# Kernel optimization log

Hardware: AMD Instinct MI355X
Metric: run time of the kernel (lower is better)

## Reference

```python
import jax, jax.numpy as jnp
import numpy as np


def setup_inputs() -> dict:
    key = jax.random.key(0)
    k1, k2 = jax.random.split(key)
    B, Tq, Tk, D = 8, 2048, 2048, 1024
    decoder_hidden = jax.random.normal(k1, (B, Tq, D), dtype=jnp.float32)
    encoder_outputs = jax.random.normal(k2, (B, Tk, D), dtype=jnp.float32)
    return {"decoder_hidden": decoder_hidden, "encoder_outputs": encoder_outputs}


def reference(decoder_hidden, encoder_outputs):
    # scores: [B, Tq, Tk] = decoder_hidden @ encoder_outputs^T (no scaling, as in source)
    scores = jnp.einsum("bqd,bkd->bqk", decoder_hidden, encoder_outputs)
    attention_weights = jax.nn.softmax(scores, axis=2)
    # context: [B, Tq, D]
    context_vector = jnp.einsum("bqk,bkd->bqd", attention_weights, encoder_outputs)
    return (context_vector, attention_weights)
```

## Files before the change

### kernel.cpp

```cpp
#include <hip/hip_runtime.h>


typedef _Float16 f16;
typedef _Float16 half4 __attribute__((ext_vector_type(4)));
typedef _Float16 half8 __attribute__((ext_vector_type(8)));
typedef float floatx16 __attribute__((ext_vector_type(16)));

#define BM 128
#define BN 128
#define BK 64

__device__ __forceinline__ void gl2lds16(const void* g, void* l) {
    __builtin_amdgcn_global_load_lds(
        (const __attribute__((address_space(1))) unsigned int*)g,
        (__attribute__((address_space(3))) unsigned int*)l,
        16, 0, 0);
}

__global__ __launch_bounds__(256) void cvt_f32_f16(const float* __restrict__ src,
                                                   f16* __restrict__ dst, int n4) {
    int i = blockIdx.x * 256 + threadIdx.x;
    if (i >= n4) return;
    float4 v = ((const float4*)src)[i];
    half4 h;
    h[0] = (f16)v.x; h[1] = (f16)v.y; h[2] = (f16)v.z; h[3] = (f16)v.w;
    ((half4*)dst)[i] = h;
}

__global__ __launch_bounds__(256) void k_cvt_transpose(const float* __restrict__ K,
                                                       f16* __restrict__ Kh,
                                                       f16* __restrict__ Kt) {
    __shared__ f16 tile[64][72];
    const int b  = blockIdx.z;
    const int k0 = blockIdx.y * 64;
    const int d0 = blockIdx.x * 64;
    const float* src = K + (size_t)b * 2048 * 1024;
    f16* khb = Kh + (size_t)b * 2048 * 1024;
    f16* ktb = Kt + (size_t)b * 1024 * 2048;
    const int r  = threadIdx.x >> 4;
    const int c4 = (threadIdx.x & 15) * 4;
    #pragma unroll
    for (int it = 0; it < 4; it++) {
        int kr = it * 16 + r;
        float4 v = *(const float4*)&src[(size_t)(k0 + kr) * 1024 + d0 + c4];
        half4 h;
        h[0] = (f16)v.x; h[1] = (f16)v.y; h[2] = (f16)v.z; h[3] = (f16)v.w;
        *(half4*)&khb[(size_t)(k0 + kr) * 1024 + d0 + c4] = h;
        *(half4*)&tile[kr][c4] = h;
    }
    __syncthreads();
    #pragma unroll
    for (int it = 0; it < 4; it++) {
        int dr = it * 16 + r;
        half4 h;
        h[0] = tile[c4 + 0][dr]; h[1] = tile[c4 + 1][dr];
        h[2] = tile[c4 + 2][dr]; h[3] = tile[c4 + 3][dr];
        *(half4*)&ktb[(size_t)(d0 + dr) * 2048 + k0 + c4] = h;
    }
}

__global__ __launch_bounds__(256) void gemm_bt(const f16* __restrict__ Amat,
                                               const f16* __restrict__ Bmat,
                                               float* __restrict__ C,
                                               int K_, int N, int nN,
                                               long sA, long sB, long sC) {
    __shared__ f16 As[BM * BK];
    __shared__ f16 Bs[BN * BK];
    const int tid  = threadIdx.x;
    const int lane = tid & 63;
    const int wave = tid >> 6;
    const int wm = (wave & 1) * 64;
    const int wn = (wave >> 1) * 64;
    const int bz = blockIdx.x;
    const int tileM = (blockIdx.y / nN) * BM;
    const int tileN = (blockIdx.y % nN) * BN;
    const f16* Ab = Amat + (size_t)bz * sA;
    const f16* Bb = Bmat + (size_t)bz * sB;
    float* Cb = C + (size_t)bz * sC;

    floatx16 acc[2][2];
    #pragma unroll
    for (int t = 0; t < 2; t++)
        #pragma unroll
        for (int u = 0; u < 2; u++)
            #pragma unroll
            for (int r = 0; r < 16; r++) acc[t][u][r] = 0.f;

    const int l31 = lane & 31;
    const int khalf = lane >> 5;
    const int sw = lane & 7;

    for (int k0 = 0; k0 < K_; k0 += BK) {
        #pragma unroll
        for (int r = 0; r < 4; r++) {
            int h = r * 256 + tid;
            int row = h >> 3, cc = h & 7;
            int gcc = cc ^ (row & 7);
            gl2lds16(Ab + (size_t)(tileM + row) * K_ + k0 + gcc * 8, &As[h * 8]);
        }
        #pragma unroll
        for (int r = 0; r < 4; r++) {
            int h = r * 256 + tid;
            int row = h >> 3, cc = h & 7;
            int gcc = cc ^ (row & 7);
            gl2lds16(Bb + (size_t)(tileN + row) * K_ + k0 + gcc * 8, &Bs[h * 8]);
        }
        __syncthreads();

        #pragma unroll
        for (int s = 0; s < 4; s++) {
            const int pc = (s * 2 + khalf) ^ sw;
            half8 af[2], bf[2];
            #pragma unroll
            for (int t = 0; t < 2; t++)
                af[t] = *(const half8*)&As[(wm + t * 32 + l31) * BK + pc * 8];
            #pragma unroll
            for (int u = 0; u < 2; u++)
                bf[u] = *(const half8*)&Bs[(wn + u * 32 + l31) * BK + pc * 8];
            #pragma unroll
            for (int t = 0; t < 2; t++)
                #pragma unroll
                for (int u = 0; u < 2; u++)
                    acc[t][u] = __builtin_amdgcn_mfma_f32_32x32x16_f16(af[t], bf[u], acc[t][u], 0, 0, 0);
        }
        __syncthreads();
    }

    #pragma unroll
    for (int t = 0; t < 2; t++) {
        #pragma unroll
        for (int u = 0; u < 2; u++) {
            int col = tileN + wn + u * 32 + l31;
            int rbase = tileM + wm + t * 32 + 4 * khalf;
            #pragma unroll
            for (int r = 0; r < 16; r++) {
                int row = rbase + (r & 3) + 8 * (r >> 2);
                Cb[(size_t)row * N + col] = acc[t][u][r];
            }
        }
    }
}

__global__ __launch_bounds__(256) void softmax_rows(float* __restrict__ S,
                                                    f16* __restrict__ Wh) {
    const size_t row = blockIdx.x;
    float* p = S + row * 2048;
    f16* ph = Wh + row * 2048;
    const int tid = threadIdx.x;
    const int lane = tid & 63;
    const int wave = tid >> 6;
    __shared__ float red[8];

    float4 va = ((const float4*)p)[tid];
    float4 vb = ((const float4*)p)[tid + 256];
    float m = fmaxf(fmaxf(fmaxf(va.x, va.y), fmaxf(va.z, va.w)),
                    fmaxf(fmaxf(vb.x, vb.y), fmaxf(vb.z, vb.w)));
    #pragma unroll
    for (int off = 32; off; off >>= 1) m = fmaxf(m, __shfl_xor(m, off));
    if (lane == 0) red[wave] = m;
    __syncthreads();
    m = fmaxf(fmaxf(red[0], red[1]), fmaxf(red[2], red[3]));

    va.x = __expf(va.x - m); va.y = __expf(va.y - m);
    va.z = __expf(va.z - m); va.w = __expf(va.w - m);
    vb.x = __expf(vb.x - m); vb.y = __expf(vb.y - m);
    vb.z = __expf(vb.z - m); vb.w = __expf(vb.w - m);
    float s = va.x + va.y + va.z + va.w + vb.x + vb.y + vb.z + vb.w;
    #pragma unroll
    for (int off = 32; off; off >>= 1) s += __shfl_xor(s, off);
    if (lane == 0) red[4 + wave] = s;
    __syncthreads();
    s = red[4] + red[5] + red[6] + red[7];
    float inv = 1.0f / s;
    va.x *= inv; va.y *= inv; va.z *= inv; va.w *= inv;
    vb.x *= inv; vb.y *= inv; vb.z *= inv; vb.w *= inv;
    ((float4*)p)[tid] = va;
    ((float4*)p)[tid + 256] = vb;
    half4 ha, hb;
    ha[0] = (f16)va.x; ha[1] = (f16)va.y; ha[2] = (f16)va.z; ha[3] = (f16)va.w;
    hb[0] = (f16)vb.x; hb[1] = (f16)vb.y; hb[2] = (f16)vb.z; hb[3] = (f16)vb.w;
    ((half4*)ph)[tid] = ha;
    ((half4*)ph)[tid + 256] = hb;
}

extern "C" void kernel_launch(void* const* d_in, const int* in_sizes, int n_in,
                              void* d_out, int out_size, void* d_ws, size_t ws_size,
                              hipStream_t stream) {
    const float* Q = (const float*)d_in[0];
    const float* K = (const float*)d_in[1];
    float* ctx = (float*)d_out;
    float* W   = (float*)d_out + 16777216;

    f16* Qh = (f16*)d_ws;
    f16* Kh = Qh + 16777216;
    f16* Kt = Kh + 16777216;
    f16* Wh = (f16*)d_ws;

    cvt_f32_f16<<<16384, 256, 0, stream>>>(Q, Qh, 4194304);
    k_cvt_transpose<<<dim3(16, 32, 8), 256, 0, stream>>>(K, Kh, Kt);

    gemm_bt<<<dim3(8, 256), 256, 0, stream>>>(
        Qh, Kh, W, 1024, 2048, 16, 2048L * 1024, 2048L * 1024, 2048L * 2048);

    softmax_rows<<<16384, 256, 0, stream>>>(W, Wh);

    gemm_bt<<<dim3(8, 128), 256, 0, stream>>>(
        Wh, Kt, ctx, 2048, 1024, 8, 2048L * 2048, 1024L * 2048, 2048L * 1024);
}
```

Before: 479.9 us.

## Replace GEMM with 256x256 tile, 8-wave, double-buffered pipelined MFMA kernel

```diff
diff --git a/kernel.cpp b/kernel.cpp
--- a/kernel.cpp
+++ b/kernel.cpp
@@ -5,10 +5,6 @@
 typedef _Float16 half4 __attribute__((ext_vector_type(4)));
 typedef _Float16 half8 __attribute__((ext_vector_type(8)));
 typedef float floatx16 __attribute__((ext_vector_type(16)));
-
-#define BM 128
-#define BN 128
-#define BK 64
 
 __device__ __forceinline__ void gl2lds16(const void* g, void* l) {
     __builtin_amdgcn_global_load_lds(
@@ -16,6 +12,8 @@
         (__attribute__((address_space(3))) unsigned int*)l,
         16, 0, 0);
 }
+
+#define MFMA(a, b, c) __builtin_amdgcn_mfma_f32_32x32x16_f16((a), (b), (c), 0, 0, 0)
 
 __global__ __launch_bounds__(256) void cvt_f32_f16(const float* __restrict__ src,
                                                    f16* __restrict__ dst, int n4) {
@@ -59,83 +57,155 @@
     }
 }
 
-__global__ __launch_bounds__(256) void gemm_bt(const f16* __restrict__ Amat,
-                                               const f16* __restrict__ Bmat,
-                                               float* __restrict__ C,
-                                               int K_, int N, int nN,
-                                               long sA, long sB, long sC) {
-    __shared__ f16 As[BM * BK];
-    __shared__ f16 Bs[BN * BK];
+__global__ __launch_bounds__(512) void gemm_bt8(const f16* __restrict__ Amat,
+                                                const f16* __restrict__ Bmat,
+                                                float* __restrict__ C,
+                                                int K_, int N, int nN,
+                                                long sA, long sB, long sC) {
+    __shared__ __align__(16) f16 LA[2][2][8192];
+    __shared__ __align__(16) f16 LB[2][2][8192];
     const int tid  = threadIdx.x;
     const int lane = tid & 63;
     const int wave = tid >> 6;
-    const int wm = (wave & 1) * 64;
-    const int wn = (wave >> 1) * 64;
-    const int bz = blockIdx.x;
-    const int tileM = (blockIdx.y / nN) * BM;
-    const int tileN = (blockIdx.y % nN) * BN;
+    const int wm   = wave >> 2;
+    const int wn   = wave & 3;
+    const int bz   = blockIdx.x;
+    const int tileM = (blockIdx.y / nN) * 256;
+    const int tileN = (blockIdx.y % nN) * 256;
     const f16* Ab = Amat + (size_t)bz * sA;
     const f16* Bb = Bmat + (size_t)bz * sB;
     float* Cb = C + (size_t)bz * sC;
-
-    floatx16 acc[2][2];
-    #pragma unroll
-    for (int t = 0; t < 2; t++)
-        #pragma unroll
-        for (int u = 0; u < 2; u++)
+    const int NT = K_ >> 6;
+
+    const int r0  = tid >> 3;
+    const int gcc = (tid & 7) ^ (r0 & 7);
+    const f16* sAp = Ab + (size_t)(tileM + r0) * K_ + gcc * 8;
+    const f16* sBp = Bb + (size_t)(tileN + (r0 & 31) + (r0 >> 5) * 64) * K_ + gcc * 8;
+
+    const int r31 = lane & 31;
+    const int kh  = lane >> 5;
+    const int sw  = lane & 7;
+
+    floatx16 acc[4][2];
+    #pragma unroll
+    for (int f = 0; f < 4; f++)
+        #pragma unroll
+        for (int g = 0; g < 2; g++)
             #pragma unroll
-            for (int r = 0; r < 16; r++) acc[t][u][r] = 0.f;
-
-    const int l31 = lane & 31;
-    const int khalf = lane >> 5;
-    const int sw = lane & 7;
-
-    for (int k0 = 0; k0 < K_; k0 += BK) {
-        #pragma unroll
-        for (int r = 0; r < 4; r++) {
-            int h = r * 256 + tid;
-            int row = h >> 3, cc = h & 7;
-            int gcc = cc ^ (row & 7);
-            gl2lds16(Ab + (size_t)(tileM + row) * K_ + k0 + gcc * 8, &As[h * 8]);
-        }
-        #pragma unroll
-        for (int r = 0; r < 4; r++) {
-            int h = r * 256 + tid;
-            int row = h >> 3, cc = h & 7;
-            int gcc = cc ^ (row & 7);
-            gl2lds16(Bb + (size_t)(tileN + row) * K_ + k0 + gcc * 8, &Bs[h * 8]);
-        }
-        __syncthreads();
-
-        #pragma unroll
-        for (int s = 0; s < 4; s++) {
-            const int pc = (s * 2 + khalf) ^ sw;
-            half8 af[2], bf[2];
-            #pragma unroll
-            for (int t = 0; t < 2; t++)
-                af[t] = *(const half8*)&As[(wm + t * 32 + l31) * BK + pc * 8];
-            #pragma unroll
-            for (int u = 0; u < 2; u++)
-                bf[u] = *(const half8*)&Bs[(wn + u * 32 + l31) * BK + pc * 8];
-            #pragma unroll
-            for (int t = 0; t < 2; t++)
-                #pragma unroll
-                for (int u = 0; u < 2; u++)
-                    acc[t][u] = __builtin_amdgcn_mfma_f32_32x32x16_f16(af[t], bf[u], acc[t][u], 0, 0, 0);
-        }
-        __syncthreads();
-    }
-
-    #pragma unroll
-    for (int t = 0; t < 2; t++) {
-        #pragma unroll
-        for (int u = 0; u < 2; u++) {
-            int col = tileN + wn + u * 32 + l31;
-            int rbase = tileM + wm + t * 32 + 4 * khalf;
+            for (int r = 0; r < 16; r++) acc[f][g][r] = 0.f;
+
+    auto STAGE_A = [&](int par, int h, int T) {
+        const f16* s = sAp + (size_t)(h * 64) * K_ + T * 64;
+        f16* d = &LA[par][h][tid * 8];
+        gl2lds16(s, d);
+        gl2lds16(s + (size_t)128 * K_, d + 4096);
+    };
+    auto STAGE_B = [&](int par, int h, int T) {
+        const f16* s = sBp + (size_t)(h * 32) * K_ + T * 64;
+        f16* d = &LB[par][h][tid * 8];
+        gl2lds16(s, d);
+        gl2lds16(s + (size_t)128 * K_, d + 4096);
+    };
+    auto LDA = [&](int par, int f, int ks) -> half8 {
+        int lr = ((f & 1) << 5) + r31 + (wm << 6);
+        int pc = ((ks << 1) + kh) ^ sw;
+        return *(const half8*)&LA[par][f >> 1][lr * 64 + pc * 8];
+    };
+    auto LDB = [&](int par, int g, int ks) -> half8 {
+        int lr = (wn << 5) + r31;
+        int pc = ((ks << 1) + kh) ^ sw;
+        return *(const half8*)&LB[par][g][lr * 64 + pc * 8];
+    };
+
+    STAGE_A(0, 0, 0); STAGE_B(0, 0, 0); STAGE_A(0, 1, 0); STAGE_B(0, 1, 0);
+    STAGE_A(1, 0, 1); STAGE_B(1, 0, 1); STAGE_A(1, 1, 1);
+    asm volatile("s_waitcnt vmcnt(6)" ::: "memory");
+    __builtin_amdgcn_s_barrier();
+
+    half8 af[2][4], bfa[4], bfb[4];
+    for (int T = 0; T < NT; ++T) {
+        const int par = T & 1, nxt = par ^ 1;
+        #pragma unroll
+        for (int ks = 0; ks < 4; ks++) {
+            af[0][ks] = LDA(par, 0, ks);
+            af[1][ks] = LDA(par, 1, ks);
+            bfa[ks]   = LDB(par, 0, ks);
+        }
+        if (T + 1 < NT) STAGE_B(nxt, 1, T + 1);
+        asm volatile("s_waitcnt lgkmcnt(8)" ::: "memory");
+        __builtin_amdgcn_s_barrier();
+        asm volatile("s_waitcnt lgkmcnt(0)" ::: "memory");
+        __builtin_amdgcn_sched_barrier(0);
+        __builtin_amdgcn_s_setprio(1);
+        #pragma unroll
+        for (int ks = 0; ks < 4; ks++) {
+            acc[0][0] = MFMA(af[0][ks], bfa[ks], acc[0][0]);
+            acc[1][0] = MFMA(af[1][ks], bfa[ks], acc[1][0]);
+        }
+        __builtin_amdgcn_s_setprio(0);
+        __builtin_amdgcn_sched_barrier(0);
+        __builtin_amdgcn_s_barrier();
+        #pragma unroll
+        for (int ks = 0; ks < 4; ks++) bfb[ks] = LDB(par, 1, ks);
+        if (T + 2 < NT) STAGE_A(par, 0, T + 2);
+        __builtin_amdgcn_s_barrier();
+        asm volatile("s_waitcnt lgkmcnt(0)" ::: "memory");
+        __builtin_amdgcn_sched_barrier(0);
+        __builtin_amdgcn_s_setprio(1);
+        #pragma unroll
+        for (int ks = 0; ks < 4; ks++) {
+            acc[0][1] = MFMA(af[0][ks], bfb[ks], acc[0][1]);
+            acc[1][1] = MFMA(af[1][ks], bfb[ks], acc[1][1]);
+        }
+        __builtin_amdgcn_s_setprio(0);
+        __builtin_amdgcn_sched_barrier(0);
+        __builtin_amdgcn_s_barrier();
+        #pragma unroll
+        for (int ks = 0; ks < 4; ks++) {
+            af[0][ks] = LDA(par, 2, ks);
+            af[1][ks] = LDA(par, 3, ks);
+        }
+        if (T + 2 < NT) STAGE_B(par, 0, T + 2);
+        __builtin_amdgcn_s_barrier();
+        asm volatile("s_waitcnt lgkmcnt(0)" ::: "memory");
+        __builtin_amdgcn_sched_barrier(0);
+        __builtin_amdgcn_s_setprio(1);
+        #pragma unroll
+        for (int ks = 0; ks < 4; ks++) {
+            acc[2][1] = MFMA(af[0][ks], bfb[ks], acc[2][1]);
+            acc[3][1] = MFMA(af[1][ks], bfb[ks], acc[3][1]);
+        }
+        __builtin_amdgcn_s_setprio(0);
+        __builtin_amdgcn_sched_barrier(0);
+        __builtin_amdgcn_s_barrier();
+        if (T + 2 < NT) {
+            STAGE_A(par, 1, T + 2);
+            asm volatile("s_waitcnt vmcnt(6)" ::: "memory");
+        } else {
+            asm volatile("s_waitcnt vmcnt(0)" ::: "memory");
+        }
+        __builtin_amdgcn_s_barrier();
+        __builtin_amdgcn_s_setprio(1);
+        #pragma unroll
+        for (int ks = 0; ks < 4; ks++) {
+            acc[2][0] = MFMA(af[0][ks], bfa[ks], acc[2][0]);
+            acc[3][0] = MFMA(af[1][ks], bfa[ks], acc[3][0]);
+        }
+        __builtin_amdgcn_s_setprio(0);
+        __builtin_amdgcn_sched_barrier(0);
+        __builtin_amdgcn_s_barrier();
+    }
+
+    #pragma unroll
+    for (int f = 0; f < 4; f++) {
+        #pragma unroll
+        for (int g = 0; g < 2; g++) {
+            int col   = tileN + (wn << 6) + (g << 5) + r31;
+            int rbase = tileM + (wm << 7) + (f << 5) + (kh << 2);
             #pragma unroll
             for (int r = 0; r < 16; r++) {
-                int row = rbase + (r & 3) + 8 * (r >> 2);
-                Cb[(size_t)row * N + col] = acc[t][u][r];
+                int row = rbase + (r & 3) + ((r >> 2) << 3);
+                Cb[(size_t)row * N + col] = acc[f][g][r];
             }
         }
     }
@@ -199,11 +269,11 @@
     cvt_f32_f16<<<16384, 256, 0, stream>>>(Q, Qh, 4194304);
     k_cvt_transpose<<<dim3(16, 32, 8), 256, 0, stream>>>(K, Kh, Kt);
 
-    gemm_bt<<<dim3(8, 256), 256, 0, stream>>>(
-        Qh, Kh, W, 1024, 2048, 16, 2048L * 1024, 2048L * 1024, 2048L * 2048);
+    gemm_bt8<<<dim3(8, 64), 512, 0, stream>>>(
+        Qh, Kh, W, 1024, 2048, 8, 2048L * 1024, 2048L * 1024, 2048L * 2048);
 
     softmax_rows<<<16384, 256, 0, stream>>>(W, Wh);
 
-    gemm_bt<<<dim3(8, 128), 256, 0, stream>>>(
-        Wh, Kt, ctx, 2048, 1024, 8, 2048L * 2048, 1024L * 2048, 2048L * 1024);
-}
+    gemm_bt8<<<dim3(8, 32), 512, 0, stream>>>(
+        Wh, Kt, ctx, 2048, 1024, 4, 2048L * 2048, 1024L * 2048, 2048L * 1024);
+}
```

New measurement: 476.7 us. Within noise of the previous version (-0.7%).

## Replace GEMM with 256x256-tile 8-wave double-buffered pipelined MFMA kernel

Applied to the files above, without the earlier changes.

```diff
diff --git a/kernel.cpp b/kernel.cpp
--- a/kernel.cpp
+++ b/kernel.cpp
@@ -5,10 +5,6 @@
 typedef _Float16 half4 __attribute__((ext_vector_type(4)));
 typedef _Float16 half8 __attribute__((ext_vector_type(8)));
 typedef float floatx16 __attribute__((ext_vector_type(16)));
-
-#define BM 128
-#define BN 128
-#define BK 64
 
 __device__ __forceinline__ void gl2lds16(const void* g, void* l) {
     __builtin_amdgcn_global_load_lds(
@@ -16,6 +12,25 @@
         (__attribute__((address_space(3))) unsigned int*)l,
         16, 0, 0);
 }
+
+__device__ __forceinline__ unsigned lds_off(const void* p) {
+    return (unsigned)(unsigned long long)
+        (const __attribute__((address_space(3))) void*)p;
+}
+
+__device__ __forceinline__ half8 dsr(unsigned a) {
+    half8 r;
+    asm volatile("ds_read_b128 %0, %1" : "=v"(r) : "v"(a));
+    return r;
+}
+
+#define MFMA(a, b, c) __builtin_amdgcn_mfma_f32_32x32x16_f16((a), (b), (c), 0, 0, 0)
+#define WAIT_LGKM0() asm volatile("s_waitcnt lgkmcnt(0)" ::: "memory")
+#define WAIT_LGKM8() asm volatile("s_waitcnt lgkmcnt(8)" ::: "memory")
+#define WAIT_VM6()   asm volatile("s_waitcnt vmcnt(6)" ::: "memory")
+#define WAIT_VM0()   asm volatile("s_waitcnt vmcnt(0)" ::: "memory")
+#define SBAR()       __builtin_amdgcn_s_barrier()
+#define SCHED0()     __builtin_amdgcn_sched_barrier(0)
 
 __global__ __launch_bounds__(256) void cvt_f32_f16(const float* __restrict__ src,
                                                    f16* __restrict__ dst, int n4) {
@@ -59,86 +74,158 @@
     }
 }
 
-__global__ __launch_bounds__(256) void gemm_bt(const f16* __restrict__ Amat,
-                                               const f16* __restrict__ Bmat,
-                                               float* __restrict__ C,
-                                               int K_, int N, int nN,
-                                               long sA, long sB, long sC) {
-    __shared__ f16 As[BM * BK];
-    __shared__ f16 Bs[BN * BK];
+__global__ __launch_bounds__(512, 2) void gemm_bt8(const f16* __restrict__ Amat,
+                                                   const f16* __restrict__ Bmat,
+                                                   float* __restrict__ C,
+                                                   int K_, int N, int nN,
+                                                   long sA, long sB, long sC) {
+    __shared__ __align__(16) f16 LA[2][2][8192];
+    __shared__ __align__(16) f16 LB[2][2][8192];
     const int tid  = threadIdx.x;
     const int lane = tid & 63;
     const int wave = tid >> 6;
-    const int wm = (wave & 1) * 64;
-    const int wn = (wave >> 1) * 64;
-    const int bz = blockIdx.x;
-    const int tileM = (blockIdx.y / nN) * BM;
-    const int tileN = (blockIdx.y % nN) * BN;
+    const int wm   = wave >> 2;
+    const int wn   = wave & 3;
+    const int bz   = blockIdx.x;
+    const int tileM = (blockIdx.y / nN) * 256;
+    const int tileN = (blockIdx.y % nN) * 256;
     const f16* Ab = Amat + (size_t)bz * sA;
     const f16* Bb = Bmat + (size_t)bz * sB;
     float* Cb = C + (size_t)bz * sC;
-
-    floatx16 acc[2][2];
-    #pragma unroll
-    for (int t = 0; t < 2; t++)
-        #pragma unroll
-        for (int u = 0; u < 2; u++)
-            #pragma unroll
-            for (int r = 0; r < 16; r++) acc[t][u][r] = 0.f;
-
-    const int l31 = lane & 31;
-    const int khalf = lane >> 5;
-    const int sw = lane & 7;
-
-    for (int k0 = 0; k0 < K_; k0 += BK) {
-        #pragma unroll
-        for (int r = 0; r < 4; r++) {
-            int h = r * 256 + tid;
-            int row = h >> 3, cc = h & 7;
-            int gcc = cc ^ (row & 7);
-            gl2lds16(Ab + (size_t)(tileM + row) * K_ + k0 + gcc * 8, &As[h * 8]);
+    const int NT = K_ >> 6;
+    const size_t g2 = (size_t)128 * K_;
+
+    const int r0  = tid >> 3;
+    const int gcc = (tid & 7) ^ (r0 & 7);
+    const f16* sAp = Ab + (size_t)(tileM + r0) * K_ + gcc * 8;
+    const f16* sBp = Bb + (size_t)(tileN + (r0 & 31) + (r0 >> 5) * 64) * K_ + gcc * 8;
+
+    const int r31 = lane & 31;
+    const int kh  = lane >> 5;
+    const int sw  = lane & 7;
+    const unsigned baseA0 = lds_off(&LA[0][0][0]) + (unsigned)((r31 + (wm << 6)) * 128);
+    const unsigned baseB0 = lds_off(&LB[0][0][0]) + (unsigned)(((wn << 5) + r31) * 128);
+    const unsigned pc0 = (unsigned)(((0 + kh) ^ sw) << 4);
+    const unsigned pc1 = (unsigned)(((2 + kh) ^ sw) << 4);
+    const unsigned pc2 = (unsigned)(((4 + kh) ^ sw) << 4);
+    const unsigned pc3 = (unsigned)(((6 + kh) ^ sw) << 4);
+
+    floatx16 acc00 = {0.f}, acc01 = {0.f}, acc10 = {0.f}, acc11 = {0.f};
+    floatx16 acc20 = {0.f}, acc21 = {0.f}, acc30 = {0.f}, acc31 = {0.f};
+    #pragma unroll
+    for (int r = 0; r < 16; r++) {
+        acc00[r] = 0.f; acc01[r] = 0.f; acc10[r] = 0.f; acc11[r] = 0.f;
+        acc20[r] = 0.f; acc21[r] = 0.f; acc30[r] = 0.f; acc31[r] = 0.f;
+    }
+
+#define STAGE_A(P, H, SRC) do { const f16* _s = (SRC); f16* _d = &LA[P][H][tid * 8]; \
+        gl2lds16(_s, _d); gl2lds16(_s + g2, _d + 4096); } while (0)
+#define STAGE_B(P, H, SRC) do { const f16* _s = (SRC); f16* _d = &LB[P][H][tid * 8]; \
+        gl2lds16(_s, _d); gl2lds16(_s + g2, _d + 4096); } while (0)
+
+    STAGE_A(0, 0, sAp);
+    STAGE_B(0, 0, sBp);
+    STAGE_A(0, 1, sAp + (size_t)64 * K_);
+    STAGE_B(0, 1, sBp + (size_t)32 * K_);
+    STAGE_A(1, 0, sAp + 64);
+    STAGE_B(1, 0, sBp + 64);
+    STAGE_A(1, 1, sAp + (size_t)64 * K_ + 64);
+    WAIT_VM6();
+    SBAR();
+
+    const f16* gB1 = sBp + (size_t)32 * K_ + 64;
+    const f16* gA0 = sAp + 128;
+    const f16* gB0 = sBp + 128;
+    const f16* gA1 = sAp + (size_t)64 * K_ + 128;
+
+    for (int T = 0; T < NT; ++T) {
+        const int par = T & 1;
+        const unsigned bA = baseA0 + (unsigned)(par << 15);
+        const unsigned bB = baseB0 + (unsigned)(par << 15);
+
+        half8 a00 = dsr(bA + pc0),        a01 = dsr(bA + pc1);
+        half8 a02 = dsr(bA + pc2),        a03 = dsr(bA + pc3);
+        half8 a10 = dsr(bA + 4096 + pc0), a11 = dsr(bA + 4096 + pc1);
+        half8 a12 = dsr(bA + 4096 + pc2), a13 = dsr(bA + 4096 + pc3);
+        half8 b00 = dsr(bB + pc0),        b01 = dsr(bB + pc1);
+        half8 b02 = dsr(bB + pc2),        b03 = dsr(bB + pc3);
+        if (T + 1 < NT) STAGE_B(par ^ 1, 1, gB1);
+        WAIT_LGKM8();
+        SBAR();
+        WAIT_LGKM0();
+        SCHED0();
+        __builtin_amdgcn_s_setprio(1);
+        acc00 = MFMA(a00, b00, acc00); acc10 = MFMA(a10, b00, acc10);
+        acc00 = MFMA(a01, b01, acc00); acc10 = MFMA(a11, b01, acc10);
+        acc00 = MFMA(a02, b02, acc00); acc10 = MFMA(a12, b02, acc10);
+        acc00 = MFMA(a03, b03, acc00); acc10 = MFMA(a13, b03, acc10);
+        __builtin_amdgcn_s_setprio(0);
+        SCHED0();
+        SBAR();
+        half8 b10 = dsr(bB + 16384 + pc0), b11 = dsr(bB + 16384 + pc1);
+        half8 b12 = dsr(bB + 16384 + pc2), b13 = dsr(bB + 16384 + pc3);
+        if (T + 2 < NT) STAGE_A(par, 0, gA0);
+        SBAR();
+        WAIT_LGKM0();
+        SCHED0();
+        __builtin_amdgcn_s_setprio(1);
+        acc01 = MFMA(a00, b10, acc01); acc11 = MFMA(a10, b10, acc11);
+        acc01 = MFMA(a01, b11, acc01); acc11 = MFMA(a11, b11, acc11);
+        acc01 = MFMA(a02, b12, acc01); acc11 = MFMA(a12, b12, acc11);
+        acc01 = MFMA(a03, b13, acc01); acc11 = MFMA(a13, b13, acc11);
+        __builtin_amdgcn_s_setprio(0);
+        SCHED0();
+        SBAR();
+        half8 a20 = dsr(bA + 16384 + pc0),        a21 = dsr(bA + 16384 + pc1);
+        half8 a22 = dsr(bA + 16384 + pc2),        a23 = dsr(bA + 16384 + pc3);
+        half8 a30 = dsr(bA + 20480 + pc0),        a31 = dsr(bA + 20480 + pc1);
+        half8 a32 = dsr(bA + 20480 + pc2),        a33 = dsr(bA + 20480 + pc3);
+        if (T + 2 < NT) STAGE_B(par, 0, gB0);
+        SBAR();
+        WAIT_LGKM0();
+        SCHED0();
+        __builtin_amdgcn_s_setprio(1);
+        acc21 = MFMA(a20, b10, acc21); acc31 = MFMA(a30, b10, acc31);
+        acc21 = MFMA(a21, b11, acc21); acc31 = MFMA(a31, b11, acc31);
+        acc21 = MFMA(a22, b12, acc21); acc31 = MFMA(a32, b12, acc31);
+        acc21 = MFMA(a23, b13, acc21); acc31 = MFMA(a33, b13, acc31);
+        __builtin_amdgcn_s_setprio(0);
+        SCHED0();
+        SBAR();
+        if (T + 2 < NT) {
+            STAGE_A(par, 1, gA1);
+            WAIT_VM6();
+        } else {
+            WAIT_VM0();
         }
-        #pragma unroll
-        for (int r = 0; r < 4; r++) {
-            int h = r * 256 + tid;
-            int row = h >> 3, cc = h & 7;
-            int gcc = cc ^ (row & 7);
-            gl2lds16(Bb + (size_t)(tileN + row) * K_ + k0 + gcc * 8, &Bs[h * 8]);
-        }
-        __syncthreads();
-
-        #pragma unroll
-        for (int s = 0; s < 4; s++) {
-            const int pc = (s * 2 + khalf) ^ sw;
-            half8 af[2], bf[2];
-            #pragma unroll
-            for (int t = 0; t < 2; t++)
-                af[t] = *(const half8*)&As[(wm + t * 32 + l31) * BK + pc * 8];
-            #pragma unroll
-            for (int u = 0; u < 2; u++)
-                bf[u] = *(const half8*)&Bs[(wn + u * 32 + l31) * BK + pc * 8];
-            #pragma unroll
-            for (int t = 0; t < 2; t++)
-                #pragma unroll
-                for (int u = 0; u < 2; u++)
-                    acc[t][u] = __builtin_amdgcn_mfma_f32_32x32x16_f16(af[t], bf[u], acc[t][u], 0, 0, 0);
-        }
-        __syncthreads();
-    }
-
-    #pragma unroll
-    for (int t = 0; t < 2; t++) {
-        #pragma unroll
-        for (int u = 0; u < 2; u++) {
-            int col = tileN + wn + u * 32 + l31;
-            int rbase = tileM + wm + t * 32 + 4 * khalf;
-            #pragma unroll
-            for (int r = 0; r < 16; r++) {
-                int row = rbase + (r & 3) + 8 * (r >> 2);
-                Cb[(size_t)row * N + col] = acc[t][u][r];
-            }
-        }
-    }
+        SBAR();
+        SCHED0();
+        __builtin_amdgcn_s_setprio(1);
+        acc20 = MFMA(a20, b00, acc20); acc30 = MFMA(a30, b00, acc30);
+        acc20 = MFMA(a21, b01, acc20); acc30 = MFMA(a31, b01, acc30);
+        acc20 = MFMA(a22, b02, acc20); acc30 = MFMA(a32, b02, acc30);
+        acc20 = MFMA(a23, b03, acc20); acc30 = MFMA(a33, b03, acc30);
+        __builtin_amdgcn_s_setprio(0);
+        SCHED0();
+        SBAR();
+        gB1 += 64; gA0 += 64; gB0 += 64; gA1 += 64;
+    }
+
+#define EPI(ACC, F, G) do { \
+        int col   = tileN + (wn << 6) + ((G) << 5) + r31; \
+        int rbase = tileM + (wm << 7) + ((F) << 5) + (kh << 2); \
+        _Pragma("unroll") \
+        for (int r = 0; r < 16; r++) { \
+            int row = rbase + (r & 3) + ((r >> 2) << 3); \
+            Cb[(size_t)row * N + col] = ACC[r]; \
+        } } while (0)
+    EPI(acc00, 0, 0); EPI(acc01, 0, 1);
+    EPI(acc10, 1, 0); EPI(acc11, 1, 1);
+    EPI(acc20, 2, 0); EPI(acc21, 2, 1);
+    EPI(acc30, 3, 0); EPI(acc31, 3, 1);
+#undef EPI
+#undef STAGE_A
+#undef STAGE_B
 }
 
 __global__ __launch_bounds__(256) void softmax_rows(float* __restrict__ S,
@@ -199,11 +286,11 @@
     cvt_f32_f16<<<16384, 256, 0, stream>>>(Q, Qh, 4194304);
     k_cvt_transpose<<<dim3(16, 32, 8), 256, 0, stream>>>(K, Kh, Kt);
 
-    gemm_bt<<<dim3(8, 256), 256, 0, stream>>>(
-        Qh, Kh, W, 1024, 2048, 16, 2048L * 1024, 2048L * 1024, 2048L * 2048);
+    gemm_bt8<<<dim3(8, 64), 512, 0, stream>>>(
+        Qh, Kh, W, 1024, 2048, 8, 2048L * 1024, 2048L * 1024, 2048L * 2048);
 
     softmax_rows<<<16384, 256, 0, stream>>>(W, Wh);
 
-    gemm_bt<<<dim3(8, 128), 256, 0, stream>>>(
-        Wh, Kt, ctx, 2048, 1024, 8, 2048L * 2048, 1024L * 2048, 2048L * 1024);
-}
+    gemm_bt8<<<dim3(8, 32), 512, 0, stream>>>(
+        Wh, Kt, ctx, 2048, 1024, 4, 2048L * 2048, 1024L * 2048, 2048L * 1024);
+}
```

After: 472.8 us. About the same (-1.5%).
